# Kernel optimization log

Measured on AMD Instinct MI355X. Metric: run time of the kernel, lower is better.

Reference implementation:

```python
import jax, jax.numpy as jnp
import numpy as np

H = 32      # num_attention_heads
HD = 64     # head_dim
MD = 64     # qk_mqa_dim (rope dim)
EPS = 1e-6
SCALING = (HD + MD) ** -0.5
NEG = -1e9


def rms_norm(x, w):
    var = jnp.mean(jnp.square(x), axis=-1, keepdims=True)
    return x * jax.lax.rsqrt(var + EPS) * w


def rotate_half(x):
    x1, x2 = jnp.split(x, 2, axis=-1)
    return jnp.concatenate([-x2, x1], axis=-1)


def apply_rope(x, cos, sin):
    return x * cos + rotate_half(x) * sin


def setup_inputs() -> dict:
    key = jax.random.key(0)
    ks = jax.random.split(key, 6)
    B, S, D = 1, 2048, 2048
    QR, KVR = 1024, 896
    hidden_states = jax.random.normal(ks[0], (B, S, D), jnp.float32)
    # real rotary tables for the MD-dim rope subspace
    inv_freq = 1.0 / (10000.0 ** (np.arange(0, MD, 2, dtype=np.float32) / MD))
    freqs = np.arange(S, dtype=np.float32)[:, None] * inv_freq[None, :]
    emb = np.concatenate([freqs, freqs], axis=-1)  # [S, MD]
    cos = jnp.asarray(np.cos(emb), jnp.float32)
    sin = jnp.asarray(np.sin(emb), jnp.float32)
    s = 0.02
    Wqa = jax.random.normal(ks[1], (QR, D), jnp.float32) * s
    q_ln_w = jnp.ones((QR,), jnp.float32)
    Wqb = jax.random.normal(ks[2], (H * (HD + MD), QR), jnp.float32) * s
    Wkva = jax.random.normal(ks[3], (KVR + MD, D), jnp.float32) * s
    kv_ln_w = jnp.ones((KVR,), jnp.float32)
    Wkvb = jax.random.normal(ks[4], (2 * H * HD, KVR), jnp.float32) * s
    Wo = jax.random.normal(ks[5], (D, H * HD), jnp.float32) * s
    return {"hidden_states": hidden_states, "cos": cos, "sin": sin,
            "Wqa": Wqa, "q_ln_w": q_ln_w, "Wqb": Wqb,
            "Wkva": Wkva, "kv_ln_w": kv_ln_w, "Wkvb": Wkvb, "Wo": Wo}


def reference(hidden_states, cos, sin, Wqa, q_ln_w, Wqb, Wkva, kv_ln_w, Wkvb, Wo):
    B, S, D = hidden_states.shape
    KVR = kv_ln_w.shape[0]
    # Q: LoRA down -> RMSNorm -> up (weights pre-absorbed with rope split)
    q = rms_norm(hidden_states @ Wqa.T, q_ln_w) @ Wqb.T      # [B,S,H*(HD+MD)]
    q = q.reshape(B, S, H, HD + MD).transpose(0, 2, 1, 3)     # [B,H,S,HD+MD]
    q_nope, q_rope = q[..., :HD], q[..., HD:]
    # KV: shared compressed latent + MQA rope key
    ckv = hidden_states @ Wkva.T                               # [B,S,KVR+MD]
    kv_nope, k_rope = ckv[..., :KVR], ckv[..., KVR:]
    kv_nope = rms_norm(kv_nope, kv_ln_w)
    q_rope = apply_rope(q_rope, cos[None, None], sin[None, None])
    k_rope = apply_rope(k_rope[:, None], cos[None, None], sin[None, None])  # [B,1,S,MD]
    # up-project latent to per-head K_nope and V (interleaved per head)
    kv = (kv_nope @ Wkvb.T).reshape(B, S, H, 2 * HD).transpose(0, 2, 1, 3)  # [B,H,S,2*HD]
    k_nope, value = kv[..., :HD], kv[..., HD:]
    key_states = jnp.concatenate(
        [k_nope, jnp.broadcast_to(k_rope, (B, H, S, MD))], axis=-1)  # repeat_kv of rope part
    query_states = jnp.concatenate([q_nope, q_rope], axis=-1)        # [B,H,S,HD+MD]
    # causal SDPA with scaling = (head_dim + qk_mqa_dim)^-0.5
    scores = jnp.einsum('bhqd,bhkd->bhqk', query_states, key_states) * SCALING
    causal = jnp.tril(jnp.ones((S, S), bool))
    scores = jnp.where(causal[None, None], scores, NEG)
    probs = jax.nn.softmax(scores, axis=-1)
    out = jnp.einsum('bhqk,bhkd->bhqd', probs, value)                # [B,H,S,HD]
    out = out.transpose(0, 2, 1, 3).reshape(B, S, H * HD)
    return out @ Wo.T
```

## Files before the change

kernel.cpp:

```cpp
#include <hip/hip_runtime.h>
#include <stdint.h>

typedef unsigned short u16;
typedef __attribute__((ext_vector_type(4))) float f32x4;
typedef __attribute__((ext_vector_type(4))) unsigned short u16x4;
typedef __attribute__((ext_vector_type(8))) unsigned short u16x8;
typedef __attribute__((ext_vector_type(8))) short s16x8;
typedef __attribute__((ext_vector_type(4))) short s16x4;
typedef __attribute__((ext_vector_type(2))) unsigned int u32x2;

#define DEVI static __device__ __forceinline__

DEVI u16 f2b(float f) {
  union { float f; unsigned u; } v; v.f = f;
  unsigned r = v.u + 0x7fffu + ((v.u >> 16) & 1u);
  return (u16)(r >> 16);
}
DEVI float b2f(u16 b) {
  union { unsigned u; float f; } v; v.u = ((unsigned)b) << 16;
  return v.f;
}

DEVI void gload_lds16(const void* gptr, void* lptr) {
  typedef const __attribute__((address_space(1))) unsigned gq;
  typedef __attribute__((address_space(3))) unsigned lq;
  __builtin_amdgcn_global_load_lds((gq*)(uintptr_t)gptr,
                                   (lq*)(uint32_t)(uintptr_t)lptr, 16, 0, 0);
}

DEVI unsigned cvtpk(float a, float b) {
  unsigned d;
  asm("v_cvt_pk_bf16_f32 %0, %1, %2" : "=v"(d) : "v"(a), "v"(b));
  return d;
}
DEVI f32x4 mfma16(s16x4 a, s16x4 b, f32x4 c) {
  f32x4 d;
  asm("v_mfma_f32_16x16x16_bf16 %0, %1, %2, %3" : "=v"(d) : "v"(a), "v"(b), "v"(c));
  return d;
}
DEVI float exp2a(float x) {
  float d;
  asm("v_exp_f32 %0, %1" : "=v"(d) : "v"(x));
  return d;
}

__global__ __launch_bounds__(256) void cvt_all(
    const float* __restrict__ X, const float* __restrict__ Wqa,
    const float* __restrict__ Wkva, const float* __restrict__ Wqb,
    const float* __restrict__ Wkvb, const float* __restrict__ Wo,
    u16* __restrict__ Xb, u16* __restrict__ W1, u16* __restrict__ Wqbb,
    u16* __restrict__ Wkvbb, u16* __restrict__ Wob) {
  int i = blockIdx.x * 256 + threadIdx.x;
  const int stride = gridDim.x * 256;
  for (; i < 5079040; i += stride) {
    const float* s; u16* d; int j;
    if (i < 1572864) {
      if (i < 1048576) { s = X; d = Xb; j = i; }
      else             { s = Wqa; d = W1; j = i - 1048576; }
    } else if (i < 3112960) {
      if (i < 2064384) { s = Wkva; d = W1 + 1024 * 2048; j = i - 1572864; }
      else             { s = Wqb; d = Wqbb; j = i - 2064384; }
    } else {
      if (i < 4030464) { s = Wkvb; d = Wkvbb; j = i - 3112960; }
      else             { s = Wo; d = Wob; j = i - 4030464; }
    }
    f32x4 v = *(const f32x4*)(s + (size_t)j * 4);
    u16x4 o;
    o[0] = f2b(v[0]); o[1] = f2b(v[1]); o[2] = f2b(v[2]); o[3] = f2b(v[3]);
    *(u16x4*)(d + (size_t)j * 4) = o;
  }
}

#define GEMM_STAGE(AP, BP, KK, k0, buf)                                        \
  {                                                                            \
    _Pragma("unroll") for (int p = 0; p < 4; ++p) {                            \
      const int c = tid + p * 256;                                             \
      gload_lds16(AP + (size_t)(m0 + (c >> 3)) * (KK) + (k0) + (c & 7) * 8,    \
                  &As[buf][c * 8]);                                            \
    }                                                                          \
    _Pragma("unroll") for (int p = 0; p < 4; ++p) {                            \
      const int c = tid + p * 256;                                             \
      gload_lds16(BP + (size_t)(n0 + (c >> 3)) * (KK) + (k0) + (c & 7) * 8,    \
                  &Bs[buf][c * 8]);                                            \
    }                                                                          \
  }

#define GEMM_COMPUTE(cur)                                                      \
  _Pragma("unroll") for (int kk = 0; kk < 64; kk += 32) {                      \
    s16x8 af[4], bfr[4];                                                       \
    _Pragma("unroll") for (int i = 0; i < 4; ++i)                              \
      af[i] = *(const s16x8*)&As[cur][(wm * 64 + i * 16 + c15) * 64 + kk + g * 8]; \
    _Pragma("unroll") for (int i = 0; i < 4; ++i)                              \
      bfr[i] = *(const s16x8*)&Bs[cur][(wn * 64 + i * 16 + c15) * 64 + kk + g * 8]; \
    _Pragma("unroll") for (int i = 0; i < 4; ++i)                              \
      _Pragma("unroll") for (int j = 0; j < 4; ++j)                            \
        acc[i][j] = __builtin_amdgcn_mfma_f32_16x16x32_bf16(af[i], bfr[j],     \
                                                            acc[i][j], 0, 0, 0); \
  }

__global__ __launch_bounds__(256) void gemm_f32(const u16* __restrict__ A,
                                                const u16* __restrict__ B,
                                                float* __restrict__ C,
                                                int M, int N, int K) {
  __shared__ __align__(16) u16 As[2][128 * 64];
  __shared__ __align__(16) u16 Bs[2][128 * 64];
  const int tid = threadIdx.x;
  const int lane = tid & 63, w = tid >> 6;
  const int wm = w >> 1, wn = w & 1;
  const int c15 = lane & 15, g = lane >> 4;
  const int m0 = blockIdx.y * 128, n0 = blockIdx.x * 128;
  f32x4 acc[4][4] = {};

  GEMM_STAGE(A, B, K, 0, 0);
  __syncthreads();
  const int nk = K >> 6;
  for (int kt = 0; kt < nk; ++kt) {
    const int cur = kt & 1;
    if (kt + 1 < nk) GEMM_STAGE(A, B, K, (kt + 1) << 6, cur ^ 1);
    GEMM_COMPUTE(cur);
    __syncthreads();
  }
#pragma unroll
  for (int i = 0; i < 4; ++i)
#pragma unroll
    for (int j = 0; j < 4; ++j) {
      const int mr = m0 + wm * 64 + i * 16 + g * 4;
      const int nc = n0 + wn * 64 + j * 16 + c15;
#pragma unroll
      for (int r = 0; r < 4; ++r)
        C[(size_t)(mr + r) * N + nc] = acc[i][j][r];
    }
}

__global__ __launch_bounds__(256) void gemm2_fused(
    const u16* __restrict__ qn, const u16* __restrict__ Wqbb,
    const u16* __restrict__ kvn, const u16* __restrict__ Wkvbb,
    u16* __restrict__ qraw, char* __restrict__ KbB, char* __restrict__ VtB) {
  __shared__ __align__(16) u16 As[2][128 * 64];
  __shared__ __align__(16) u16 Bs[2][128 * 64];
  const int z = blockIdx.z;
  const u16* A = z ? kvn : qn;
  const u16* B = z ? Wkvbb : Wqbb;
  const int K = z ? 896 : 1024;
  const int tid = threadIdx.x;
  const int lane = tid & 63, w = tid >> 6;
  const int wm = w >> 1, wn = w & 1;
  const int c15 = lane & 15, g = lane >> 4;
  const int m0 = blockIdx.y * 128, n0 = blockIdx.x * 128;
  f32x4 acc[4][4] = {};

  GEMM_STAGE(A, B, K, 0, 0);
  __syncthreads();
  const int nk = K >> 6;
  for (int kt = 0; kt < nk; ++kt) {
    const int cur = kt & 1;
    if (kt + 1 < nk) GEMM_STAGE(A, B, K, (kt + 1) << 6, cur ^ 1);
    GEMM_COMPUTE(cur);
    __syncthreads();
  }

  if (z == 0) {
#pragma unroll
    for (int i = 0; i < 4; ++i)
#pragma unroll
      for (int j = 0; j < 4; ++j) {
        const int mr = m0 + wm * 64 + i * 16 + g * 4;
        const int nc = n0 + wn * 64 + j * 16 + c15;
#pragma unroll
        for (int r = 0; r < 4; ++r)
          qraw[(size_t)(mr + r) * 4096 + nc] = f2b(acc[i][j][r]);
      }
  } else {
    const int h = n0 >> 7;
#pragma unroll
    for (int i = 0; i < 4; ++i)
#pragma unroll
      for (int j = 0; j < 4; ++j) {
        const int mr = m0 + wm * 64 + i * 16 + g * 4;
        if (wn == 0) {
          const int d = j * 16 + c15;
#pragma unroll
          for (int r = 0; r < 4; ++r) {
            const int s = mr + r;
            *(u16*)(KbB + ((size_t)(h * 2048 + s) << 8) +
                    ((2 * d) ^ ((s & 7) << 4))) = f2b(acc[i][j][r]);
          }
        } else {
          const int d = j * 16 + c15;
          u16x4 o;
#pragma unroll
          for (int r = 0; r < 4; ++r) o[r] = f2b(acc[i][j][r]);
          *(u16x4*)(VtB + ((size_t)(h * 64 + d) << 12) +
                    ((2 * mr) ^ ((d & 7) << 4))) = o;
        }
      }
  }
}

DEVI float block_sum(float v, float* sbuf, int tid) {
#pragma unroll
  for (int o = 32; o; o >>= 1) v += __shfl_xor(v, o, 64);
  __syncthreads();
  if ((tid & 63) == 0) sbuf[tid >> 6] = v;
  __syncthreads();
  return sbuf[0] + sbuf[1] + sbuf[2] + sbuf[3];
}

__global__ __launch_bounds__(256) void norm_rope(const float* __restrict__ C1,
    const float* __restrict__ qw, const float* __restrict__ kw,
    const float* __restrict__ cosb, const float* __restrict__ sinb,
    u16* __restrict__ qn, u16* __restrict__ kvn, char* __restrict__ KbB) {
  __shared__ float sbuf[4];
  __shared__ __align__(16) u16 rv[64];
  const int s = blockIdx.x, tid = threadIdx.x;
  const float* row = C1 + (size_t)s * 2048;

  f32x4 qv = *(const f32x4*)(row + tid * 4);
  float ss = qv[0]*qv[0] + qv[1]*qv[1] + qv[2]*qv[2] + qv[3]*qv[3];
  ss = block_sum(ss, sbuf, tid);
  const float scale = rsqrtf(ss * (1.f / 1024.f) + 1e-6f);
  {
    f32x4 wv = *(const f32x4*)(qw + tid * 4);
    u16x4 o;
#pragma unroll
    for (int j = 0; j < 4; ++j) o[j] = f2b(qv[j] * scale * wv[j]);
    *(u16x4*)(qn + (size_t)s * 1024 + tid * 4) = o;
  }

  float ss2 = 0.f;
  f32x4 kvv = {};
  if (tid < 224) {
    kvv = *(const f32x4*)(row + 1024 + tid * 4);
    ss2 = kvv[0]*kvv[0] + kvv[1]*kvv[1] + kvv[2]*kvv[2] + kvv[3]*kvv[3];
  }
  ss2 = block_sum(ss2, sbuf, tid);
  const float sc2 = rsqrtf(ss2 * (1.f / 896.f) + 1e-6f);
  if (tid < 224) {
    f32x4 wv = *(const f32x4*)(kw + tid * 4);
    u16x4 o;
#pragma unroll
    for (int j = 0; j < 4; ++j) o[j] = f2b(kvv[j] * sc2 * wv[j]);
    *(u16x4*)(kvn + (size_t)s * 896 + tid * 4) = o;
  }

  if (tid < 64) {
    const int d = tid;
    const float x = row[1920 + d];
    const float part = row[1920 + (d < 32 ? d + 32 : d - 32)];
    const float cv = cosb[s * 64 + d], sv = sinb[s * 64 + d];
    rv[d] = f2b(d < 32 ? (x * cv - part * sv) : (x * cv + part * sv));
  }
  __syncthreads();
  {
    const int h = tid >> 3, c8 = tid & 7;
    const u16x8 v = *(const u16x8*)&rv[c8 * 8];
    *(u16x8*)(KbB + ((size_t)(h * 2048 + s) << 8) +
              ((128 + c8 * 16) ^ ((s & 7) << 4))) = v;
  }
}

__global__ __launch_bounds__(256) void attn_fwd(
    const u16* __restrict__ Qb, const u16* __restrict__ Kb,
    const u16* __restrict__ Vt, const float* __restrict__ cosb,
    const float* __restrict__ sinb, u16* __restrict__ attn) {
  __shared__ __align__(16) u16 Klds[2][64 * 128];
  __shared__ __align__(16) u16 Vlds[2][64 * 64];
  const int tid = threadIdx.x;
  const int lane = tid & 63, w = tid >> 6;
  const int c15 = lane & 15, g = lane >> 4;
  const int orig = blockIdx.x;
  const int l = (orig & 7) * 128 + (orig >> 3);
  const int h = l >> 5;
  const int qb = 31 - (l & 31);
  const int qrow = qb * 64 + w * 16 + c15;
  const char* KbHB = (const char*)Kb + ((size_t)h << 19);
  const char* VtHB = (const char*)Vt + ((size_t)h << 18);
  const float SC2 = 0.12753860478587782f;

  s16x8 qf[4];
  {
    const u16* qp = Qb + (size_t)qrow * 4096 + h * 128;
    u16x8 x0 = *(const u16x8*)(qp + g * 8);
    u16x8 x1 = *(const u16x8*)(qp + 32 + g * 8);
    u16x8 x2 = *(const u16x8*)(qp + 64 + g * 8);
    u16x8 x3 = *(const u16x8*)(qp + 96 + g * 8);
    const float* cb = cosb + (size_t)qrow * 64 + g * 8;
    const float* sb = sinb + (size_t)qrow * 64 + g * 8;
#pragma unroll
    for (int i = 0; i < 8; ++i) {
      qf[0][i] = (short)f2b(b2f(x0[i]) * SC2);
      qf[1][i] = (short)f2b(b2f(x1[i]) * SC2);
      const float f2 = b2f(x2[i]), f3 = b2f(x3[i]);
      qf[2][i] = (short)f2b((f2 * cb[i] - f3 * sb[i]) * SC2);
      qf[3][i] = (short)f2b((f3 * cb[32 + i] + f2 * sb[32 + i]) * SC2);
    }
  }

  const int nt = qb + 1;
  auto STAGE = [&](int t, int buf) {
    const int kv0 = t << 6;
#pragma unroll
    for (int p = 0; p < 4; ++p) {
      const int c = tid + p * 256;
      gload_lds16(KbHB + ((size_t)(kv0 + (c >> 4)) << 8) + (c & 15) * 16,
                  (char*)Klds[buf] + c * 16);
    }
#pragma unroll
    for (int p = 0; p < 2; ++p) {
      const int c = tid + p * 256;
      gload_lds16(VtHB + ((size_t)(c >> 3) << 12) + 2 * kv0 + (c & 7) * 16,
                  (char*)Vlds[buf] + c * 16);
    }
  };

  f32x4 acc[4] = {};
  float m = -1e9f, ssum = 0.f;

  STAGE(0, 0);
  __syncthreads();

  for (int t = 0; t < nt; ++t) {
    const int cur = t & 1;
    const int kv0 = t << 6;
    if (t + 1 < nt) STAGE(t + 1, cur ^ 1);

    const u16* Kc = Klds[cur];
    const u16* Vc = Vlds[cur];

    float pv[4][4];
    float pm = -1e9f;
    __builtin_amdgcn_s_setprio(1);
#pragma unroll
    for (int kvh = 0; kvh < 4; ++kvh) {
      f32x4 s4 = {};
      const int rb = (kvh * 16 + c15) * 256;
#pragma unroll
      for (int d0 = 0; d0 < 4; ++d0) {
        s16x8 kf = *(const s16x8*)((const char*)Kc + rb +
                                   ((d0 * 64 + g * 16) ^ ((c15 & 7) << 4)));
        s4 = __builtin_amdgcn_mfma_f32_16x16x32_bf16(kf, qf[d0], s4, 0, 0, 0);
      }
      pv[kvh][0] = s4[0]; pv[kvh][1] = s4[1];
      pv[kvh][2] = s4[2]; pv[kvh][3] = s4[3];
    }
    __builtin_amdgcn_s_setprio(0);
    if (t == nt - 1) {
#pragma unroll
      for (int kvh = 0; kvh < 4; ++kvh)
#pragma unroll
        for (int r = 0; r < 4; ++r) {
          const int kv = kv0 + kvh * 16 + g * 4 + r;
          if (kv > qrow) pv[kvh][r] = -1e9f;
        }
    }
#pragma unroll
    for (int kvh = 0; kvh < 4; ++kvh)
#pragma unroll
      for (int r = 0; r < 4; ++r) pm = fmaxf(pm, pv[kvh][r]);
    pm = fmaxf(pm, __shfl_xor(pm, 16, 64));
    pm = fmaxf(pm, __shfl_xor(pm, 32, 64));
    if (!__all(pm - m <= 8.f)) {
      const float mnew = fmaxf(m, pm);
      const float alpha = exp2a(m - mnew);
      ssum *= alpha;
#pragma unroll
      for (int dt = 0; dt < 4; ++dt) acc[dt] *= alpha;
      m = mnew;
    }
    float rs = 0.f;
#pragma unroll
    for (int kvh = 0; kvh < 4; ++kvh)
#pragma unroll
      for (int r = 0; r < 4; ++r) {
        const float p = exp2a(pv[kvh][r] - m);
        pv[kvh][r] = p;
        rs += p;
      }
    rs += __shfl_xor(rs, 16, 64);
    rs += __shfl_xor(rs, 32, 64);
    ssum += rs;

    s16x4 pB[4];
#pragma unroll
    for (int ks = 0; ks < 4; ++ks) {
      u32x2 pw;
      pw[0] = cvtpk(pv[ks][0], pv[ks][1]);
      pw[1] = cvtpk(pv[ks][2], pv[ks][3]);
      pB[ks] = __builtin_bit_cast(s16x4, pw);
    }
    __builtin_amdgcn_s_setprio(1);
#pragma unroll
    for (int dt = 0; dt < 4; ++dt) {
      const int rb2 = (dt * 16 + c15) * 128;
#pragma unroll
      for (int ks = 0; ks < 4; ++ks) {
        s16x4 vf = *(const s16x4*)((const char*)Vc + rb2 +
                                   ((ks * 32 + g * 8) ^ ((c15 & 7) << 4)));
        acc[dt] = mfma16(vf, pB[ks], acc[dt]);
      }
    }
    __builtin_amdgcn_s_setprio(0);
    __syncthreads();
  }

  const float inv = 1.f / ssum;
#pragma unroll
  for (int dt = 0; dt < 4; ++dt) {
    u16x4 o;
#pragma unroll
    for (int r = 0; r < 4; ++r) o[r] = f2b(acc[dt][r] * inv);
    *(u16x4*)(attn + (size_t)qrow * 2048 + h * 64 + dt * 16 + g * 4) = o;
  }
}

extern "C" void kernel_launch(void* const* d_in, const int* in_sizes, int n_in,
                              void* d_out, int out_size, void* d_ws, size_t ws_size,
                              hipStream_t stream) {
  const float* X    = (const float*)d_in[0];
  const float* cosb = (const float*)d_in[1];
  const float* sinb = (const float*)d_in[2];
  const float* Wqa  = (const float*)d_in[3];
  const float* qlnw = (const float*)d_in[4];
  const float* Wqb  = (const float*)d_in[5];
  const float* Wkva = (const float*)d_in[6];
  const float* klnw = (const float*)d_in[7];
  const float* Wkvb = (const float*)d_in[8];
  const float* Wo   = (const float*)d_in[9];
  float* out = (float*)d_out;
  char* ws = (char*)d_ws;

  u16*   Xb     = (u16*)(ws + 0);
  u16*   W1     = (u16*)(ws + 8388608);
  float* C1     = (float*)(ws + 16777216);
  u16*   qn     = (u16*)(ws + 33554432);
  u16*   kvn    = (u16*)(ws + 37748736);
  u16*   Wqbb   = (u16*)(ws + 41943040);
  u16*   Wkvbb  = (u16*)(ws + 50331648);
  u16*   qraw_b = (u16*)(ws + 0);
  u16*   Kb     = (u16*)(ws + 58720256);
  u16*   VtG    = (u16*)(ws + 75497472);
  u16*   attnb  = (u16*)(ws + 83886080);
  u16*   Wob    = (u16*)(ws + 92274688);

  cvt_all<<<2048, 256, 0, stream>>>(X, Wqa, Wkva, Wqb, Wkvb, Wo,
                                    Xb, W1, Wqbb, Wkvbb, Wob);

  gemm_f32<<<dim3(16, 16), 256, 0, stream>>>(Xb, W1, C1, 2048, 2048, 2048);

  norm_rope<<<2048, 256, 0, stream>>>(C1, qlnw, klnw, cosb, sinb, qn, kvn, (char*)Kb);

  gemm2_fused<<<dim3(32, 16, 2), 256, 0, stream>>>(qn, Wqbb, kvn, Wkvbb,
                                                   qraw_b, (char*)Kb, (char*)VtG);

  attn_fwd<<<1024, 256, 0, stream>>>(qraw_b, Kb, VtG, cosb, sinb, attnb);

  gemm_f32<<<dim3(16, 16), 256, 0, stream>>>(attnb, Wob, out, 2048, 2048, 2048);
}
```

Baseline: 206.6 us.

## Use 8-wave blocks for GEMMs and attention with 128-row query tiles

All GEMM kernels now run with 512 threads (8 waves in a 2x4 layout) over the same 128x128 tile, so each wave holds a 64x32 accumulator instead of 64x64. The attention kernel moves to 128-row query blocks with 8 waves, so one K/V tile in LDS is shared by twice as many query rows. Per-wave work on fully masked KV tiles is skipped, the causal mask is applied only on diagonal tiles, and block-to-head mapping pairs short and long query blocks per XCD. This aims to improve latency hiding and K/V reuse, at the cost of more barrier participants and idle waves in diagonal tiles.

```diff
diff --git a/kernel.cpp b/kernel.cpp
--- a/kernel.cpp
+++ b/kernel.cpp
@@ -71,68 +71,73 @@
   }
 }
 
-#define GEMM_STAGE(AP, BP, KK, k0, buf)                                        \
+#define GEMM8_STAGE(AP, BP, KK, k0, buf)                                       \
   {                                                                            \
-    _Pragma("unroll") for (int p = 0; p < 4; ++p) {                            \
-      const int c = tid + p * 256;                                             \
+    _Pragma("unroll") for (int p = 0; p < 2; ++p) {                            \
+      const int c = tid + p * 512;                                             \
       gload_lds16(AP + (size_t)(m0 + (c >> 3)) * (KK) + (k0) + (c & 7) * 8,    \
                   &As[buf][c * 8]);                                            \
     }                                                                          \
-    _Pragma("unroll") for (int p = 0; p < 4; ++p) {                            \
-      const int c = tid + p * 256;                                             \
+    _Pragma("unroll") for (int p = 0; p < 2; ++p) {                            \
+      const int c = tid + p * 512;                                             \
       gload_lds16(BP + (size_t)(n0 + (c >> 3)) * (KK) + (k0) + (c & 7) * 8,    \
                   &Bs[buf][c * 8]);                                            \
     }                                                                          \
   }
 
-#define GEMM_COMPUTE(cur)                                                      \
+#define GEMM8_COMPUTE(cur)                                                     \
   _Pragma("unroll") for (int kk = 0; kk < 64; kk += 32) {                      \
-    s16x8 af[4], bfr[4];                                                       \
+    s16x8 af[4], bfr[2];                                                       \
     _Pragma("unroll") for (int i = 0; i < 4; ++i)                              \
       af[i] = *(const s16x8*)&As[cur][(wm * 64 + i * 16 + c15) * 64 + kk + g * 8]; \
+    _Pragma("unroll") for (int j = 0; j < 2; ++j)                              \
+      bfr[j] = *(const s16x8*)&Bs[cur][(wn * 32 + j * 16 + c15) * 64 + kk + g * 8]; \
     _Pragma("unroll") for (int i = 0; i < 4; ++i)                              \
-      bfr[i] = *(const s16x8*)&Bs[cur][(wn * 64 + i * 16 + c15) * 64 + kk + g * 8]; \
-    _Pragma("unroll") for (int i = 0; i < 4; ++i)                              \
-      _Pragma("unroll") for (int j = 0; j < 4; ++j)                            \
+      _Pragma("unroll") for (int j = 0; j < 2; ++j)                            \
         acc[i][j] = __builtin_amdgcn_mfma_f32_16x16x32_bf16(af[i], bfr[j],     \
                                                             acc[i][j], 0, 0, 0); \
   }
 
-__global__ __launch_bounds__(256) void gemm_f32(const u16* __restrict__ A,
+#define GEMM8_PROLOG                                                           \
+  const int tid = threadIdx.x;                                                 \
+  const int lane = tid & 63, w = tid >> 6;                                     \
+  const int wm = w >> 2, wn = w & 3;                                           \
+  const int c15 = lane & 15, g = lane >> 4;                                    \
+  const int m0 = blockIdx.y * 128, n0 = blockIdx.x * 128;                      \
+  f32x4 acc[4][2] = {};
+
+#define GEMM8_LOOP(AP, BP, KK)                                                 \
+  GEMM8_STAGE(AP, BP, KK, 0, 0);                                               \
+  __syncthreads();                                                             \
+  const int nk = (KK) >> 6;                                                    \
+  for (int kt = 0; kt < nk; ++kt) {                                            \
+    const int cur = kt & 1;                                                    \
+    if (kt + 1 < nk) GEMM8_STAGE(AP, BP, KK, (kt + 1) << 6, cur ^ 1);          \
+    GEMM8_COMPUTE(cur);                                                        \
+    __syncthreads();                                                           \
+  }
+
+__global__ __launch_bounds__(512) void gemm_f32(const u16* __restrict__ A,
                                                 const u16* __restrict__ B,
                                                 float* __restrict__ C,
                                                 int M, int N, int K) {
   __shared__ __align__(16) u16 As[2][128 * 64];
   __shared__ __align__(16) u16 Bs[2][128 * 64];
-  const int tid = threadIdx.x;
-  const int lane = tid & 63, w = tid >> 6;
-  const int wm = w >> 1, wn = w & 1;
-  const int c15 = lane & 15, g = lane >> 4;
-  const int m0 = blockIdx.y * 128, n0 = blockIdx.x * 128;
-  f32x4 acc[4][4] = {};
-
-  GEMM_STAGE(A, B, K, 0, 0);
-  __syncthreads();
-  const int nk = K >> 6;
-  for (int kt = 0; kt < nk; ++kt) {
-    const int cur = kt & 1;
-    if (kt + 1 < nk) GEMM_STAGE(A, B, K, (kt + 1) << 6, cur ^ 1);
-    GEMM_COMPUTE(cur);
-    __syncthreads();
-  }
+  GEMM8_PROLOG
+  GEMM8_LOOP(A, B, K)
 #pragma unroll
   for (int i = 0; i < 4; ++i)
 #pragma unroll
-    for (int j = 0; j < 4; ++j) {
+    for (int j = 0; j < 2; ++j) {
       const int mr = m0 + wm * 64 + i * 16 + g * 4;
-      const int nc = n0 + wn * 64 + j * 16 + c15;
+      const int nc = n0 + wn * 32 + j * 16 + c15;
 #pragma unroll
       for (int r = 0; r < 4; ++r)
         C[(size_t)(mr + r) * N + nc] = acc[i][j][r];
     }
 }
 
-__global__ __launch_bounds__(256) void gemm2_fused(
+__global__ __launch_bounds__(512) void gemm2_fused(
     const u16* __restrict__ qn, const u16* __restrict__ Wqbb,
     const u16* __restrict__ kvn, const u16* __restrict__ Wkvbb,
     u16* __restrict__ qraw, char* __restrict__ KbB, char* __restrict__ VtB) {
@@ -142,30 +147,16 @@
   const u16* A = z ? kvn : qn;
   const u16* B = z ? Wkvbb : Wqbb;
   const int K = z ? 896 : 1024;
-  const int tid = threadIdx.x;
-  const int lane = tid & 63, w = tid >> 6;
-  const int wm = w >> 1, wn = w & 1;
-  const int c15 = lane & 15, g = lane >> 4;
-  const int m0 = blockIdx.y * 128, n0 = blockIdx.x * 128;
-  f32x4 acc[4][4] = {};
-
-  GEMM_STAGE(A, B, K, 0, 0);
-  __syncthreads();
-  const int nk = K >> 6;
-  for (int kt = 0; kt < nk; ++kt) {
-    const int cur = kt & 1;
-    if (kt + 1 < nk) GEMM_STAGE(A, B, K, (kt + 1) << 6, cur ^ 1);
-    GEMM_COMPUTE(cur);
-    __syncthreads();
-  }
+  GEMM8_PROLOG
+  GEMM8_LOOP(A, B, K)
 
   if (z == 0) {
 #pragma unroll
     for (int i = 0; i < 4; ++i)
 #pragma unroll
-      for (int j = 0; j < 4; ++j) {
+      for (int j = 0; j < 2; ++j) {
         const int mr = m0 + wm * 64 + i * 16 + g * 4;
-        const int nc = n0 + wn * 64 + j * 16 + c15;
+        const int nc = n0 + wn * 32 + j * 16 + c15;
 #pragma unroll
         for (int r = 0; r < 4; ++r)
           qraw[(size_t)(mr + r) * 4096 + nc] = f2b(acc[i][j][r]);
@@ -175,10 +166,11 @@
 #pragma unroll
     for (int i = 0; i < 4; ++i)
 #pragma unroll
-      for (int j = 0; j < 4; ++j) {
+      for (int j = 0; j < 2; ++j) {
         const int mr = m0 + wm * 64 + i * 16 + g * 4;
-        if (wn == 0) {
-          const int d = j * 16 + c15;
+        const int col = wn * 32 + j * 16 + c15;
+        if (col < 64) {
+          const int d = col;
 #pragma unroll
           for (int r = 0; r < 4; ++r) {
             const int s = mr + r;
@@ -186,7 +178,7 @@
                     ((2 * d) ^ ((s & 7) << 4))) = f2b(acc[i][j][r]);
           }
         } else {
-          const int d = j * 16 + c15;
+          const int d = col - 64;
           u16x4 o;
 #pragma unroll
           for (int r = 0; r < 4; ++r) o[r] = f2b(acc[i][j][r]);
@@ -259,7 +251,7 @@
   }
 }
 
-__global__ __launch_bounds__(256) void attn_fwd(
+__global__ __launch_bounds__(512) void attn_fwd(
     const u16* __restrict__ Qb, const u16* __restrict__ Kb,
     const u16* __restrict__ Vt, const float* __restrict__ cosb,
     const float* __restrict__ sinb, u16* __restrict__ attn) {
@@ -269,10 +261,13 @@
   const int lane = tid & 63, w = tid >> 6;
   const int c15 = lane & 15, g = lane >> 4;
   const int orig = blockIdx.x;
-  const int l = (orig & 7) * 128 + (orig >> 3);
-  const int h = l >> 5;
-  const int qb = 31 - (l & 31);
-  const int qrow = qb * 64 + w * 16 + c15;
+  const int xcd = orig & 7, l = orig >> 3;
+  const int pr = l >> 1, side = l & 1;
+  const int h = xcd * 4 + (pr >> 3);
+  const int j8 = pr & 7;
+  const int qb = side ? j8 : 15 - j8;
+  const int wmin = qb * 128 + w * 16;
+  const int qrow = wmin + c15;
   const char* KbHB = (const char*)Kb + ((size_t)h << 19);
   const char* VtHB = (const char*)Vt + ((size_t)h << 18);
   const float SC2 = 0.12753860478587782f;
@@ -296,21 +291,17 @@
     }
   }
 
-  const int nt = qb + 1;
+  const int nt = 2 * qb + 2;
   auto STAGE = [&](int t, int buf) {
     const int kv0 = t << 6;
 #pragma unroll
-    for (int p = 0; p < 4; ++p) {
-      const int c = tid + p * 256;
+    for (int p = 0; p < 2; ++p) {
+      const int c = tid + p * 512;
       gload_lds16(KbHB + ((size_t)(kv0 + (c >> 4)) << 8) + (c & 15) * 16,
                   (char*)Klds[buf] + c * 16);
     }
-#pragma unroll
-    for (int p = 0; p < 2; ++p) {
-      const int c = tid + p * 256;
-      gload_lds16(VtHB + ((size_t)(c >> 3) << 12) + 2 * kv0 + (c & 7) * 16,
-                  (char*)Vlds[buf] + c * 16);
-    }
+    gload_lds16(VtHB + ((size_t)(tid >> 3) << 12) + 2 * kv0 + (tid & 7) * 16,
+                (char*)Vlds[buf] + tid * 16);
   };
 
   f32x4 acc[4] = {};
@@ -324,82 +315,84 @@
     const int kv0 = t << 6;
     if (t + 1 < nt) STAGE(t + 1, cur ^ 1);
 
-    const u16* Kc = Klds[cur];
-    const u16* Vc = Vlds[cur];
-
-    float pv[4][4];
-    float pm = -1e9f;
-    __builtin_amdgcn_s_setprio(1);
-#pragma unroll
-    for (int kvh = 0; kvh < 4; ++kvh) {
-      f32x4 s4 = {};
-      const int rb = (kvh * 16 + c15) * 256;
-#pragma unroll
-      for (int d0 = 0; d0 < 4; ++d0) {
-        s16x8 kf = *(const s16x8*)((const char*)Kc + rb +
-                                   ((d0 * 64 + g * 16) ^ ((c15 & 7) << 4)));
-        s4 = __builtin_amdgcn_mfma_f32_16x16x32_bf16(kf, qf[d0], s4, 0, 0, 0);
-      }
-      pv[kvh][0] = s4[0]; pv[kvh][1] = s4[1];
-      pv[kvh][2] = s4[2]; pv[kvh][3] = s4[3];
+    if (kv0 <= wmin + 15) {
+      const u16* Kc = Klds[cur];
+      const u16* Vc = Vlds[cur];
+
+      float pv[4][4];
+      float pm = -1e9f;
+      __builtin_amdgcn_s_setprio(1);
+#pragma unroll
+      for (int kvh = 0; kvh < 4; ++kvh) {
+        f32x4 s4 = {};
+        const int rb = (kvh * 16 + c15) * 256;
+#pragma unroll
+        for (int d0 = 0; d0 < 4; ++d0) {
+          s16x8 kf = *(const s16x8*)((const char*)Kc + rb +
+                                     ((d0 * 64 + g * 16) ^ ((c15 & 7) << 4)));
+          s4 = __builtin_amdgcn_mfma_f32_16x16x32_bf16(kf, qf[d0], s4, 0, 0, 0);
+        }
+        pv[kvh][0] = s4[0]; pv[kvh][1] = s4[1];
+        pv[kvh][2] = s4[2]; pv[kvh][3] = s4[3];
+      }
+      __builtin_amdgcn_s_setprio(0);
+      if (kv0 + 63 > wmin) {
+#pragma unroll
+        for (int kvh = 0; kvh < 4; ++kvh)
+#pragma unroll
+          for (int r = 0; r < 4; ++r) {
+            const int kv = kv0 + kvh * 16 + g * 4 + r;
+            if (kv > qrow) pv[kvh][r] = -1e9f;
+          }
+      }
+#pragma unroll
+      for (int kvh = 0; kvh < 4; ++kvh)
+#pragma unroll
+        for (int r = 0; r < 4; ++r) pm = fmaxf(pm, pv[kvh][r]);
+      pm = fmaxf(pm, __shfl_xor(pm, 16, 64));
+      pm = fmaxf(pm, __shfl_xor(pm, 32, 64));
+      if (!__all(pm - m <= 8.f)) {
+        const float mnew = fmaxf(m, pm);
+        const float alpha = exp2a(m - mnew);
+        ssum *= alpha;
+#pragma unroll
+        for (int dt = 0; dt < 4; ++dt) acc[dt] *= alpha;
+        m = mnew;
+      }
+      float rs = 0.f;
+#pragma unroll
+      for (int kvh = 0; kvh < 4; ++kvh)
+#pragma unroll
+        for (int r = 0; r < 4; ++r) {
+          const float p = exp2a(pv[kvh][r] - m);
+          pv[kvh][r] = p;
+          rs += p;
+        }
+      rs += __shfl_xor(rs, 16, 64);
+      rs += __shfl_xor(rs, 32, 64);
+      ssum += rs;
+
+      s16x4 pB[4];
+#pragma unroll
+      for (int ks = 0; ks < 4; ++ks) {
+        u32x2 pw;
+        pw[0] = cvtpk(pv[ks][0], pv[ks][1]);
+        pw[1] = cvtpk(pv[ks][2], pv[ks][3]);
+        pB[ks] = __builtin_bit_cast(s16x4, pw);
+      }
+      __builtin_amdgcn_s_setprio(1);
+#pragma unroll
+      for (int dt = 0; dt < 4; ++dt) {
+        const int rb2 = (dt * 16 + c15) * 128;
+#pragma unroll
+        for (int ks = 0; ks < 4; ++ks) {
+          s16x4 vf = *(const s16x4*)((const char*)Vc + rb2 +
+                                     ((ks * 32 + g * 8) ^ ((c15 & 7) << 4)));
+          acc[dt] = mfma16(vf, pB[ks], acc[dt]);
+        }
+      }
+      __builtin_amdgcn_s_setprio(0);
     }
-    __builtin_amdgcn_s_setprio(0);
-    if (t == nt - 1) {
-#pragma unroll
-      for (int kvh = 0; kvh < 4; ++kvh)
-#pragma unroll
-        for (int r = 0; r < 4; ++r) {
-          const int kv = kv0 + kvh * 16 + g * 4 + r;
-          if (kv > qrow) pv[kvh][r] = -1e9f;
-        }
-    }
-#pragma unroll
-    for (int kvh = 0; kvh < 4; ++kvh)
-#pragma unroll
-      for (int r = 0; r < 4; ++r) pm = fmaxf(pm, pv[kvh][r]);
-    pm = fmaxf(pm, __shfl_xor(pm, 16, 64));
-    pm = fmaxf(pm, __shfl_xor(pm, 32, 64));
-    if (!__all(pm - m <= 8.f)) {
-      const float mnew = fmaxf(m, pm);
-      const float alpha = exp2a(m - mnew);
-      ssum *= alpha;
-#pragma unroll
-      for (int dt = 0; dt < 4; ++dt) acc[dt] *= alpha;
-      m = mnew;
-    }
-    float rs = 0.f;
-#pragma unroll
-    for (int kvh = 0; kvh < 4; ++kvh)
-#pragma unroll
-      for (int r = 0; r < 4; ++r) {
-        const float p = exp2a(pv[kvh][r] - m);
-        pv[kvh][r] = p;
-        rs += p;
-      }
-    rs += __shfl_xor(rs, 16, 64);
-    rs += __shfl_xor(rs, 32, 64);
-    ssum += rs;
-
-    s16x4 pB[4];
-#pragma unroll
-    for (int ks = 0; ks < 4; ++ks) {
-      u32x2 pw;
-      pw[0] = cvtpk(pv[ks][0], pv[ks][1]);
-      pw[1] = cvtpk(pv[ks][2], pv[ks][3]);
-      pB[ks] = __builtin_bit_cast(s16x4, pw);
-    }
-    __builtin_amdgcn_s_setprio(1);
-#pragma unroll
-    for (int dt = 0; dt < 4; ++dt) {
-      const int rb2 = (dt * 16 + c15) * 128;
-#pragma unroll
-      for (int ks = 0; ks < 4; ++ks) {
-        s16x4 vf = *(const s16x4*)((const char*)Vc + rb2 +
-                                   ((ks * 32 + g * 8) ^ ((c15 & 7) << 4)));
-        acc[dt] = mfma16(vf, pB[ks], acc[dt]);
-      }
-    }
-    __builtin_amdgcn_s_setprio(0);
     __syncthreads();
   }
 
@@ -445,14 +438,14 @@
   cvt_all<<<2048, 256, 0, stream>>>(X, Wqa, Wkva, Wqb, Wkvb, Wo,
                                     Xb, W1, Wqbb, Wkvbb, Wob);
 
-  gemm_f32<<<dim3(16, 16), 256, 0, stream>>>(Xb, W1, C1, 2048, 2048, 2048);
+  gemm_f32<<<dim3(16, 16), 512, 0, stream>>>(Xb, W1, C1, 2048, 2048, 2048);
 
   norm_rope<<<2048, 256, 0, stream>>>(C1, qlnw, klnw, cosb, sinb, qn, kvn, (char*)Kb);
 
-  gemm2_fused<<<dim3(32, 16, 2), 256, 0, stream>>>(qn, Wqbb, kvn, Wkvbb,
+  gemm2_fused<<<dim3(32, 16, 2), 512, 0, stream>>>(qn, Wqbb, kvn, Wkvbb,
                                                    qraw_b, (char*)Kb, (char*)VtG);
 
-  attn_fwd<<<1024, 256, 0, stream>>>(qraw_b, Kb, VtG, cosb, sinb, attnb);
-
-  gemm_f32<<<dim3(16, 16), 256, 0, stream>>>(attnb, Wob, out, 2048, 2048, 2048);
-}
+  attn_fwd<<<512, 512, 0, stream>>>(qraw_b, Kb, VtG, cosb, sinb, attnb);
+
+  gemm_f32<<<dim3(16, 16), 512, 0, stream>>>(attnb, Wob, out, 2048, 2048, 2048);
+}
```

After: 226.6 us. +9.7%, slower.
